# Optimization experiments

Hardware: AMD Instinct MI355X
Metric: run time of the kernel (lower is better)

The kernel has to match this reference:

```python
import jax, jax.numpy as jnp
import numpy as np

N_NODES = 50000


def _sage_conv(x, src, dst, W_l, b_l, W_r, n_nodes):
    # mean-aggregate neighbor (source) features onto targets
    msg = x[src]                                   # [E, d_in] gather
    agg = jax.ops.segment_sum(msg, dst, num_segments=n_nodes)   # [N, d_in]
    deg = jax.ops.segment_sum(jnp.ones((src.shape[0],), x.dtype), dst,
                              num_segments=n_nodes)
    agg = agg / jnp.clip(deg, 1.0, None)[:, None]  # mean with deg>=1 clamp (PyG)
    # out = lin_l(agg) + lin_r(x)   (bias lives in lin_l)
    return agg @ W_l.T + b_l + x @ W_r.T


def setup_inputs() -> dict:
    key = jax.random.key(0)
    ks = jax.random.split(key, 8)
    d_in, d_hid, d_out = 128, 256, 128
    n_edges = 800000
    x = jax.random.normal(ks[0], (N_NODES, d_in), dtype=jnp.float32)
    edge_index = jax.random.randint(ks[1], (2, n_edges), 0, N_NODES, dtype=jnp.int32)
    def glorot(k, shape):
        lim = float(np.sqrt(6.0 / (shape[0] + shape[1])))
        return jax.random.uniform(k, shape, jnp.float32, -lim, lim)
    return {
        "x": x,
        "edge_index": edge_index,
        "W1l": glorot(ks[2], (d_hid, d_in)),
        "b1": jnp.zeros((d_hid,), jnp.float32),
        "W1r": glorot(ks[3], (d_hid, d_in)),
        "W2l": glorot(ks[4], (d_out, d_hid)),
        "b2": jnp.zeros((d_out,), jnp.float32),
        "W2r": glorot(ks[5], (d_out, d_hid)),
    }


def reference(x, edge_index, W1l, b1, W1r, W2l, b2, W2r):
    src, dst = edge_index[0], edge_index[1]
    h = jax.nn.relu(_sage_conv(x, src, dst, W1l, b1, W1r, N_NODES))
    out = _sage_conv(h, src, dst, W2l, b2, W2r, N_NODES)
    return out
```

## Files before the change

kernel.cpp:

```cpp
#include <hip/hip_runtime.h>
#include <hip/hip_bf16.h>

#define NN 50000
#define NN_PAD 50176
#define NE 800000
#define NB 196
#define CAP 6144
#define EPB 4096

typedef __attribute__((ext_vector_type(8))) short short8;
typedef __attribute__((ext_vector_type(4))) float f32x4;
typedef __attribute__((ext_vector_type(2))) float f32x2;

__device__ __forceinline__ unsigned short f2bf(float f) {
    union { float f; unsigned u; } v; v.f = f;
    unsigned u = v.u;
    return (unsigned short)((u + 0x7fffu + ((u >> 16) & 1u)) >> 16);
}
__device__ __forceinline__ float bfu_lo(unsigned u) {
    union { unsigned u; float f; } v; v.u = u << 16; return v.f;
}
__device__ __forceinline__ float bfu_hi(unsigned u) {
    union { unsigned u; float f; } v; v.u = u & 0xffff0000u; return v.f;
}

__global__ void k_setup_part(const float* __restrict__ W1l, const float* __restrict__ W1r,
                             const float* __restrict__ W2l, const float* __restrict__ W2r,
                             unsigned short* __restrict__ W1pk, unsigned short* __restrict__ W2pk,
                             const float4* __restrict__ x4, unsigned short* __restrict__ Abar1,
                             unsigned char* __restrict__ x_f8,
                             const int* __restrict__ src, const int* __restrict__ dst,
                             int* __restrict__ gcursor, unsigned* __restrict__ pairs) {
    int blk = blockIdx.x, t = threadIdx.x;
    if (blk < NB) {
        __shared__ int cnt[256];
        __shared__ int base[256];
        cnt[t] = 0;
        __syncthreads();
        int e0 = blk * EPB;
        int eend = min(e0 + EPB, NE);
        int rank[16], bk[16];
        unsigned pk[16];
        int m = 0;
        for (int e = e0 + t; e < eend; e += 256) {
            int s = src[e], d = dst[e];
            bk[m] = d >> 8;
            pk[m] = ((unsigned)s << 8) | (unsigned)(d & 255);
            rank[m] = atomicAdd(&cnt[bk[m]], 1);
            ++m;
        }
        __syncthreads();
        if (t < NB && cnt[t] > 0) base[t] = t * CAP + atomicAdd(&gcursor[t], cnt[t]);
        __syncthreads();
        for (int i = 0; i < m; ++i) {
            int pos = base[bk[i]] + rank[i];
            if (pos < (bk[i] + 1) * CAP) pairs[pos] = pk[i];
        }
    } else if (blk < 260) {
        int tid = (blk - 196) * 256 + t;
        int table = tid >> 13;
        int r = tid & 8191;
        int lane = r & 63, ni = (r >> 6) & 3, ks = (r >> 8) & 7, g = r >> 11;
        int lm = lane & 15, lq = lane >> 4;
        int o = g * 64 + ni * 16 + lm;
        int k = ks * 32 + lq * 8;
        unsigned short v[8];
        if (table == 0) {
            if (k < 128) {
#pragma unroll
                for (int j = 0; j < 8; ++j) v[j] = f2bf(W1l[o * 128 + k + j]);
            } else {
#pragma unroll
                for (int j = 0; j < 8; ++j) v[j] = f2bf(W1r[o * 128 + k - 128 + j]);
            }
            *(uint4*)(W1pk + (size_t)r * 8) = *(const uint4*)v;
        } else {
            if (o < 128) {
#pragma unroll
                for (int j = 0; j < 8; ++j) v[j] = f2bf(W2l[o * 256 + k + j]);
            } else {
#pragma unroll
                for (int j = 0; j < 8; ++j) v[j] = f2bf(W2r[(o - 128) * 256 + k + j]);
            }
            *(uint4*)(W2pk + (size_t)r * 8) = *(const uint4*)v;
        }
    } else {
        int gid = (blk - 260) * 256 + t;
        int n = gid >> 5, c = gid & 31;
        float4 v = x4[(size_t)n * 32 + c];
        ushort4 o;
        o.x = f2bf(v.x); o.y = f2bf(v.y); o.z = f2bf(v.z); o.w = f2bf(v.w);
        *(ushort4*)(Abar1 + (size_t)n * 256 + 128 + c * 4) = o;
        unsigned p = (unsigned)__builtin_amdgcn_cvt_pk_fp8_f32(v.x, v.y, 0, false);
        p = (unsigned)__builtin_amdgcn_cvt_pk_fp8_f32(v.z, v.w, (int)p, true);
        *(unsigned*)(x_f8 + (size_t)n * 128 + c * 4) = p;
    }
}

__global__ void k_build(const int* __restrict__ gcursor, const unsigned* __restrict__ pairs,
                        int* __restrict__ deg_i, int* __restrict__ row_start,
                        int* __restrict__ esrc) {
    __shared__ int buf[256];
    __shared__ int ldeg[256];
    __shared__ int lstart[256];
    __shared__ int sh_base, sh_cnt;
    __shared__ int lsrc[CAP];
    int b = blockIdx.x, t = threadIdx.x;
    int c = (t < NB) ? min(gcursor[t], CAP) : 0;
    buf[t] = c;
    __syncthreads();
#pragma unroll
    for (int o = 1; o < 256; o <<= 1) {
        int add = (t >= o) ? buf[t - o] : 0;
        __syncthreads();
        buf[t] += add;
        __syncthreads();
    }
    if (t == b) { sh_cnt = c; sh_base = buf[b] - c; }
    ldeg[t] = 0;
    __syncthreads();
    int cnt = sh_cnt, base = sh_base;
    int rank[CAP / 256], msrc[CAP / 256], mloc[CAP / 256];
    int m = 0;
    for (int e = t; e < cnt; e += 256) {
        unsigned p = pairs[(size_t)b * CAP + e];
        msrc[m] = (int)(p >> 8); mloc[m] = (int)(p & 255u);
        rank[m] = atomicAdd(&ldeg[mloc[m]], 1);
        ++m;
    }
    __syncthreads();
    int v = ldeg[t];
    buf[t] = v;
    __syncthreads();
#pragma unroll
    for (int o = 1; o < 256; o <<= 1) {
        int add = (t >= o) ? buf[t - o] : 0;
        __syncthreads();
        buf[t] += add;
        __syncthreads();
    }
    lstart[t] = buf[t] - v;
    int node = b * 256 + t;
    if (node < NN) { deg_i[node] = v; row_start[node] = base + lstart[t]; }
    else           { deg_i[node] = 0; row_start[node] = 0; }
    __syncthreads();
    for (int i = 0; i < m; ++i) lsrc[lstart[mloc[i]] + rank[i]] = msrc[i];
    __syncthreads();
    for (int e = t; e < cnt; e += 256) esrc[base + e] = lsrc[e];
}

__global__ void k_agg1(const uint2* __restrict__ xf8, const int* __restrict__ deg_i,
                       const int* __restrict__ row_start, const int* __restrict__ esrc,
                       unsigned short* __restrict__ Abar1) {
    int gid = blockIdx.x * blockDim.x + threadIdx.x;
    int n = gid >> 4, c = gid & 15;
    int dg = deg_i[n], st = row_start[n];
    float acc[8] = {0.f, 0.f, 0.f, 0.f, 0.f, 0.f, 0.f, 0.f};
    int i = 0;
    for (; i + 2 <= dg; i += 2) {
        int s0 = esrc[st + i], s1 = esrc[st + i + 1];
        uint2 q0 = xf8[(size_t)s0 * 16 + c];
        uint2 q1 = xf8[(size_t)s1 * 16 + c];
        f32x2 a0 = __builtin_amdgcn_cvt_pk_f32_fp8(q0.x, false);
        f32x2 a1 = __builtin_amdgcn_cvt_pk_f32_fp8(q0.x, true);
        f32x2 a2 = __builtin_amdgcn_cvt_pk_f32_fp8(q0.y, false);
        f32x2 a3 = __builtin_amdgcn_cvt_pk_f32_fp8(q0.y, true);
        f32x2 b0 = __builtin_amdgcn_cvt_pk_f32_fp8(q1.x, false);
        f32x2 b1 = __builtin_amdgcn_cvt_pk_f32_fp8(q1.x, true);
        f32x2 b2 = __builtin_amdgcn_cvt_pk_f32_fp8(q1.y, false);
        f32x2 b3 = __builtin_amdgcn_cvt_pk_f32_fp8(q1.y, true);
        acc[0] += a0.x + b0.x; acc[1] += a0.y + b0.y;
        acc[2] += a1.x + b1.x; acc[3] += a1.y + b1.y;
        acc[4] += a2.x + b2.x; acc[5] += a2.y + b2.y;
        acc[6] += a3.x + b3.x; acc[7] += a3.y + b3.y;
    }
    if (i < dg) {
        int s = esrc[st + i];
        uint2 q0 = xf8[(size_t)s * 16 + c];
        f32x2 a0 = __builtin_amdgcn_cvt_pk_f32_fp8(q0.x, false);
        f32x2 a1 = __builtin_amdgcn_cvt_pk_f32_fp8(q0.x, true);
        f32x2 a2 = __builtin_amdgcn_cvt_pk_f32_fp8(q0.y, false);
        f32x2 a3 = __builtin_amdgcn_cvt_pk_f32_fp8(q0.y, true);
        acc[0] += a0.x; acc[1] += a0.y;
        acc[2] += a1.x; acc[3] += a1.y;
        acc[4] += a2.x; acc[5] += a2.y;
        acc[6] += a3.x; acc[7] += a3.y;
    }
    float invd = 1.0f / (float)max(dg, 1);
    unsigned short o[8];
#pragma unroll
    for (int j = 0; j < 8; ++j) o[j] = f2bf(acc[j] * invd);
    *(uint4*)(Abar1 + (size_t)n * 256 + c * 8) = *(const uint4*)o;
}

__global__ __launch_bounds__(256, 2) void k_gemm12(
        const unsigned short* __restrict__ Abar1,
        const unsigned short* __restrict__ W1pk, const unsigned short* __restrict__ W2pk,
        const float* __restrict__ b1, const float* __restrict__ b2,
        unsigned char* __restrict__ y2f8, unsigned short* __restrict__ Sbf) {
    __shared__ unsigned short T[16384];
    int t = threadIdx.x, blk = blockIdx.x;
    int m0 = blk * 64;
    int wave = t >> 6, lane = t & 63;
    int lm = lane & 15, lq = lane >> 4;
    int pbase = lm * 4 + lq;

    short8 w[8][4];
    {
        const unsigned short* wb = W1pk + (size_t)wave * 16384;
#pragma unroll
        for (int ks = 0; ks < 8; ++ks)
#pragma unroll
            for (int ni = 0; ni < 4; ++ni)
                w[ks][ni] = *(const short8*)(wb + ((size_t)((ks * 4 + ni) * 64 + lane)) * 8);
    }

    {
        const uint4* gp = (const uint4*)(Abar1 + (size_t)m0 * 256);
        uint4 ld[8];
#pragma unroll
        for (int i = 0; i < 8; ++i) ld[i] = gp[i * 256 + t];
        int ks = (t >> 2) & 7, slq = t & 3;
#pragma unroll
        for (int i = 0; i < 8; ++i) {
            int mLoc = i * 8 + (t >> 5);
            int mi = mLoc >> 4, slm = mLoc & 15;
            *(uint4*)(T + ((size_t)((ks * 4 + mi) * 64 + slm * 4 + slq)) * 8) = ld[i];
        }
    }
    __syncthreads();

    f32x4 acc1[4][4];
#pragma unroll
    for (int mi = 0; mi < 4; ++mi)
#pragma unroll
        for (int ni = 0; ni < 4; ++ni) acc1[mi][ni] = (f32x4){0.f, 0.f, 0.f, 0.f};
#pragma unroll
    for (int ks = 0; ks < 8; ++ks) {
        short8 a[4];
#pragma unroll
        for (int mi = 0; mi < 4; ++mi)
            a[mi] = *(const short8*)(T + ((size_t)((ks * 4 + mi) * 64 + pbase)) * 8);
#pragma unroll
        for (int mi = 0; mi < 4; ++mi)
#pragma unroll
            for (int ni = 0; ni < 4; ++ni)
                acc1[mi][ni] = __builtin_amdgcn_mfma_f32_16x16x32_bf16(a[mi], w[ks][ni], acc1[mi][ni], 0, 0, 0);
    }

    {
        const unsigned short* wb = W2pk + (size_t)wave * 16384;
#pragma unroll
        for (int ks = 0; ks < 8; ++ks)
#pragma unroll
            for (int ni = 0; ni < 4; ++ni)
                w[ks][ni] = *(const short8*)(wb + ((size_t)((ks * 4 + ni) * 64 + lane)) * 8);
    }
    __syncthreads();

#pragma unroll
    for (int ni = 0; ni < 4; ++ni) {
        int col = wave * 64 + ni * 16 + lm;
        float bv = b1[col];
        int ks = col >> 5;
        int la = (col & 31) >> 3, j = col & 7;
#pragma unroll
        for (int mi = 0; mi < 4; ++mi)
#pragma unroll
            for (int r = 0; r < 4; ++r) {
                float v = fmaxf(acc1[mi][ni][r] + bv, 0.0f);
                T[((size_t)((ks * 4 + mi) * 64 + (lq * 4 + r) * 4 + la)) * 8 + j] = f2bf(v);
            }
    }
    __syncthreads();

    f32x4 acc2[4][4];
#pragma unroll
    for (int mi = 0; mi < 4; ++mi)
#pragma unroll
        for (int ni = 0; ni < 4; ++ni) acc2[mi][ni] = (f32x4){0.f, 0.f, 0.f, 0.f};
#pragma unroll
    for (int ks = 0; ks < 8; ++ks) {
        short8 a[4];
#pragma unroll
        for (int mi = 0; mi < 4; ++mi)
            a[mi] = *(const short8*)(T + ((size_t)((ks * 4 + mi) * 64 + pbase)) * 8);
#pragma unroll
        for (int mi = 0; mi < 4; ++mi)
#pragma unroll
            for (int ni = 0; ni < 4; ++ni)
                acc2[mi][ni] = __builtin_amdgcn_mfma_f32_16x16x32_bf16(a[mi], w[ks][ni], acc2[mi][ni], 0, 0, 0);
    }

    if (wave < 2) {
#pragma unroll
        for (int ni = 0; ni < 4; ++ni) {
            int col = wave * 64 + ni * 16 + lm;
#pragma unroll
            for (int mi = 0; mi < 4; ++mi)
#pragma unroll
                for (int r = 0; r < 4; ++r) {
                    int row = blk * 64 + mi * 16 + lq * 4 + r;
                    float v = acc2[mi][ni][r];
                    unsigned p = (unsigned)__builtin_amdgcn_cvt_pk_fp8_f32(v, v, 0, false);
                    y2f8[(size_t)row * 128 + col] = (unsigned char)(p & 0xff);
                }
        }
    } else {
#pragma unroll
        for (int ni = 0; ni < 4; ++ni) {
            int col = (wave - 2) * 64 + ni * 16 + lm;
            float bv = b2[col];
#pragma unroll
            for (int mi = 0; mi < 4; ++mi)
#pragma unroll
                for (int r = 0; r < 4; ++r) {
                    int row = blk * 64 + mi * 16 + lq * 4 + r;
                    Sbf[(size_t)row * 128 + col] = f2bf(acc2[mi][ni][r] + bv);
                }
        }
    }
}

__global__ void k_agg_out(const uint2* __restrict__ yf8, const uint4* __restrict__ Sbf4,
                          const int* __restrict__ deg_i, const int* __restrict__ row_start,
                          const int* __restrict__ esrc, float* __restrict__ out) {
    int gid = blockIdx.x * blockDim.x + threadIdx.x;
    int n = gid >> 4, c = gid & 15;
    int dg = deg_i[n], st = row_start[n];
    float acc[8] = {0.f, 0.f, 0.f, 0.f, 0.f, 0.f, 0.f, 0.f};
    int i = 0;
    for (; i + 2 <= dg; i += 2) {
        int s0 = esrc[st + i], s1 = esrc[st + i + 1];
        uint2 q0 = yf8[(size_t)s0 * 16 + c];
        uint2 q1 = yf8[(size_t)s1 * 16 + c];
        f32x2 a0 = __builtin_amdgcn_cvt_pk_f32_fp8(q0.x, false);
        f32x2 a1 = __builtin_amdgcn_cvt_pk_f32_fp8(q0.x, true);
        f32x2 a2 = __builtin_amdgcn_cvt_pk_f32_fp8(q0.y, false);
        f32x2 a3 = __builtin_amdgcn_cvt_pk_f32_fp8(q0.y, true);
        f32x2 b0 = __builtin_amdgcn_cvt_pk_f32_fp8(q1.x, false);
        f32x2 b1 = __builtin_amdgcn_cvt_pk_f32_fp8(q1.x, true);
        f32x2 b2 = __builtin_amdgcn_cvt_pk_f32_fp8(q1.y, false);
        f32x2 b3 = __builtin_amdgcn_cvt_pk_f32_fp8(q1.y, true);
        acc[0] += a0.x + b0.x; acc[1] += a0.y + b0.y;
        acc[2] += a1.x + b1.x; acc[3] += a1.y + b1.y;
        acc[4] += a2.x + b2.x; acc[5] += a2.y + b2.y;
        acc[6] += a3.x + b3.x; acc[7] += a3.y + b3.y;
    }
    if (i < dg) {
        int s = esrc[st + i];
        uint2 q0 = yf8[(size_t)s * 16 + c];
        f32x2 a0 = __builtin_amdgcn_cvt_pk_f32_fp8(q0.x, false);
        f32x2 a1 = __builtin_amdgcn_cvt_pk_f32_fp8(q0.x, true);
        f32x2 a2 = __builtin_amdgcn_cvt_pk_f32_fp8(q0.y, false);
        f32x2 a3 = __builtin_amdgcn_cvt_pk_f32_fp8(q0.y, true);
        acc[0] += a0.x; acc[1] += a0.y;
        acc[2] += a1.x; acc[3] += a1.y;
        acc[4] += a2.x; acc[5] += a2.y;
        acc[6] += a3.x; acc[7] += a3.y;
    }
    float invd = 1.0f / (float)max(dg, 1);
    uint4 sv = Sbf4[(size_t)n * 16 + c];
    float4 o0, o1;
    o0.x = bfu_lo(sv.x) + acc[0] * invd; o0.y = bfu_hi(sv.x) + acc[1] * invd;
    o0.z = bfu_lo(sv.y) + acc[2] * invd; o0.w = bfu_hi(sv.y) + acc[3] * invd;
    o1.x = bfu_lo(sv.z) + acc[4] * invd; o1.y = bfu_hi(sv.z) + acc[5] * invd;
    o1.z = bfu_lo(sv.w) + acc[6] * invd; o1.w = bfu_hi(sv.w) + acc[7] * invd;
    float* op = out + (size_t)n * 128 + c * 8;
    *(float4*)op = o0; *(float4*)(op + 4) = o1;
}

extern "C" void kernel_launch(void* const* d_in, const int* in_sizes, int n_in,
                              void* d_out, int out_size, void* d_ws, size_t ws_size,
                              hipStream_t stream) {
    const float* x   = (const float*)d_in[0];
    const int*   ei  = (const int*)d_in[1];
    const int*   src = ei;
    const int*   dst = ei + NE;
    const float* W1l = (const float*)d_in[2];
    const float* b1  = (const float*)d_in[3];
    const float* W1r = (const float*)d_in[4];
    const float* W2l = (const float*)d_in[5];
    const float* b2  = (const float*)d_in[6];
    const float* W2r = (const float*)d_in[7];
    float* out = (float*)d_out;

    char* ws = (char*)d_ws;
    int* deg_i            = (int*)(ws + 0);
    int* row_start        = (int*)(ws + 200704);
    int* gcursor          = (int*)(ws + 401408);
    int* esrc             = (int*)(ws + 409600);
    unsigned* pairs       = (unsigned*)(ws + 4194304);
    unsigned short* Sbf   = (unsigned short*)(ws + 9437184);
    unsigned char* x_f8   = (unsigned char*)(ws + 22282240);
    unsigned char* y2f8   = (unsigned char*)(ws + 28704768);
    unsigned short* Abar1 = (unsigned short*)(ws + 35651584);
    unsigned short* W1pk  = (unsigned short*)(ws + 61341696);
    unsigned short* W2pk  = (unsigned short*)(ws + 61472768);

    hipMemsetAsync(gcursor, 0, 1024, stream);
    k_setup_part<<<6510, 256, 0, stream>>>(W1l, W1r, W2l, W2r, W1pk, W2pk,
                                           (const float4*)x, Abar1, x_f8, src, dst,
                                           gcursor, pairs);
    k_build<<<NB, 256, 0, stream>>>(gcursor, pairs, deg_i, row_start, esrc);
    k_agg1<<<NN * 16 / 256, 256, 0, stream>>>((const uint2*)x_f8, deg_i, row_start, esrc, Abar1);
    k_gemm12<<<NN_PAD / 64, 256, 0, stream>>>(Abar1, W1pk, W2pk, b1, b2, y2f8, Sbf);
    k_agg_out<<<NN * 16 / 256, 256, 0, stream>>>((const uint2*)y2f8, (const uint4*)Sbf,
                                                 deg_i, row_start, esrc, out);
}
```

Baseline: 187.8 us.

## Compact CSR to 16-bit edge sources and packed start/degree metadata

Stores edge source indices as 16-bit values and packs each node's row start (20 bits) and degree (12 bits) into one word, so the aggregation kernels do one metadata load and move half the index bytes. The partition and build kernels become two-pass count-then-scatter loops with shared-memory cursors instead of keeping per-thread rank arrays in registers. The 16-bit LDS staging buffer also halves k_build's shared memory. The cost is rereading src/dst and pairs a second time, and the packing assumes node ids fit in 16 bits and degrees stay below 4096.

```diff
diff --git a/kernel.cpp b/kernel.cpp
--- a/kernel.cpp
+++ b/kernel.cpp
@@ -34,27 +34,22 @@
     int blk = blockIdx.x, t = threadIdx.x;
     if (blk < NB) {
         __shared__ int cnt[256];
+        __shared__ int cur[256];
         __shared__ int base[256];
-        cnt[t] = 0;
+        cnt[t] = 0; cur[t] = 0;
         __syncthreads();
         int e0 = blk * EPB;
         int eend = min(e0 + EPB, NE);
-        int rank[16], bk[16];
-        unsigned pk[16];
-        int m = 0;
+        for (int e = e0 + t; e < eend; e += 256)
+            atomicAdd(&cnt[dst[e] >> 8], 1);
+        __syncthreads();
+        if (t < NB && cnt[t] > 0) base[t] = t * CAP + atomicAdd(&gcursor[t], cnt[t]);
+        __syncthreads();
         for (int e = e0 + t; e < eend; e += 256) {
             int s = src[e], d = dst[e];
-            bk[m] = d >> 8;
-            pk[m] = ((unsigned)s << 8) | (unsigned)(d & 255);
-            rank[m] = atomicAdd(&cnt[bk[m]], 1);
-            ++m;
-        }
-        __syncthreads();
-        if (t < NB && cnt[t] > 0) base[t] = t * CAP + atomicAdd(&gcursor[t], cnt[t]);
-        __syncthreads();
-        for (int i = 0; i < m; ++i) {
-            int pos = base[bk[i]] + rank[i];
-            if (pos < (bk[i] + 1) * CAP) pairs[pos] = pk[i];
+            int bk = d >> 8;
+            int pos = base[bk] + atomicAdd(&cur[bk], 1);
+            if (pos < (bk + 1) * CAP) pairs[pos] = ((unsigned)s << 8) | (unsigned)(d & 255);
         }
     } else if (blk < 260) {
         int tid = (blk - 196) * 256 + t;
@@ -98,13 +93,12 @@
 }
 
 __global__ void k_build(const int* __restrict__ gcursor, const unsigned* __restrict__ pairs,
-                        int* __restrict__ deg_i, int* __restrict__ row_start,
-                        int* __restrict__ esrc) {
+                        unsigned* __restrict__ meta, unsigned short* __restrict__ esrc) {
     __shared__ int buf[256];
     __shared__ int ldeg[256];
-    __shared__ int lstart[256];
+    __shared__ int cur[256];
     __shared__ int sh_base, sh_cnt;
-    __shared__ int lsrc[CAP];
+    __shared__ unsigned short lsrc[CAP];
     int b = blockIdx.x, t = threadIdx.x;
     int c = (t < NB) ? min(gcursor[t], CAP) : 0;
     buf[t] = c;
@@ -120,41 +114,40 @@
     ldeg[t] = 0;
     __syncthreads();
     int cnt = sh_cnt, base = sh_base;
-    int rank[CAP / 256], msrc[CAP / 256], mloc[CAP / 256];
-    int m = 0;
+    for (int e = t; e < cnt; e += 256)
+        atomicAdd(&ldeg[pairs[(size_t)b * CAP + e] & 255u], 1);
+    __syncthreads();
+    int v = ldeg[t];
+    buf[t] = v;
+    __syncthreads();
+#pragma unroll
+    for (int o = 1; o < 256; o <<= 1) {
+        int add = (t >= o) ? buf[t - o] : 0;
+        __syncthreads();
+        buf[t] += add;
+        __syncthreads();
+    }
+    int lst = buf[t] - v;
+    cur[t] = lst;
+    int node = b * 256 + t;
+    meta[node] = (node < NN) ? ((unsigned)(base + lst) | ((unsigned)v << 20)) : 0u;
+    __syncthreads();
     for (int e = t; e < cnt; e += 256) {
         unsigned p = pairs[(size_t)b * CAP + e];
-        msrc[m] = (int)(p >> 8); mloc[m] = (int)(p & 255u);
-        rank[m] = atomicAdd(&ldeg[mloc[m]], 1);
-        ++m;
-    }
-    __syncthreads();
-    int v = ldeg[t];
-    buf[t] = v;
-    __syncthreads();
-#pragma unroll
-    for (int o = 1; o < 256; o <<= 1) {
-        int add = (t >= o) ? buf[t - o] : 0;
-        __syncthreads();
-        buf[t] += add;
-        __syncthreads();
-    }
-    lstart[t] = buf[t] - v;
-    int node = b * 256 + t;
-    if (node < NN) { deg_i[node] = v; row_start[node] = base + lstart[t]; }
-    else           { deg_i[node] = 0; row_start[node] = 0; }
-    __syncthreads();
-    for (int i = 0; i < m; ++i) lsrc[lstart[mloc[i]] + rank[i]] = msrc[i];
+        int pos = atomicAdd(&cur[p & 255u], 1);
+        lsrc[pos] = (unsigned short)(p >> 8);
+    }
     __syncthreads();
     for (int e = t; e < cnt; e += 256) esrc[base + e] = lsrc[e];
 }
 
-__global__ void k_agg1(const uint2* __restrict__ xf8, const int* __restrict__ deg_i,
-                       const int* __restrict__ row_start, const int* __restrict__ esrc,
+__global__ void k_agg1(const uint2* __restrict__ xf8, const unsigned* __restrict__ meta,
+                       const unsigned short* __restrict__ esrc,
                        unsigned short* __restrict__ Abar1) {
     int gid = blockIdx.x * blockDim.x + threadIdx.x;
     int n = gid >> 4, c = gid & 15;
-    int dg = deg_i[n], st = row_start[n];
+    unsigned mt = meta[n];
+    int st = (int)(mt & 0xFFFFFu), dg = (int)(mt >> 20);
     float acc[8] = {0.f, 0.f, 0.f, 0.f, 0.f, 0.f, 0.f, 0.f};
     int i = 0;
     for (; i + 2 <= dg; i += 2) {
@@ -323,11 +316,13 @@
 }
 
 __global__ void k_agg_out(const uint2* __restrict__ yf8, const uint4* __restrict__ Sbf4,
-                          const int* __restrict__ deg_i, const int* __restrict__ row_start,
-                          const int* __restrict__ esrc, float* __restrict__ out) {
+                          const unsigned* __restrict__ meta,
+                          const unsigned short* __restrict__ esrc,
+                          float* __restrict__ out) {
     int gid = blockIdx.x * blockDim.x + threadIdx.x;
     int n = gid >> 4, c = gid & 15;
-    int dg = deg_i[n], st = row_start[n];
+    unsigned mt = meta[n];
+    int st = (int)(mt & 0xFFFFFu), dg = (int)(mt >> 20);
     float acc[8] = {0.f, 0.f, 0.f, 0.f, 0.f, 0.f, 0.f, 0.f};
     int i = 0;
     for (; i + 2 <= dg; i += 2) {
@@ -386,10 +381,9 @@
     float* out = (float*)d_out;
 
     char* ws = (char*)d_ws;
-    int* deg_i            = (int*)(ws + 0);
-    int* row_start        = (int*)(ws + 200704);
+    unsigned* meta        = (unsigned*)(ws + 0);
     int* gcursor          = (int*)(ws + 401408);
-    int* esrc             = (int*)(ws + 409600);
+    unsigned short* esrc  = (unsigned short*)(ws + 409600);
     unsigned* pairs       = (unsigned*)(ws + 4194304);
     unsigned short* Sbf   = (unsigned short*)(ws + 9437184);
     unsigned char* x_f8   = (unsigned char*)(ws + 22282240);
@@ -402,9 +396,9 @@
     k_setup_part<<<6510, 256, 0, stream>>>(W1l, W1r, W2l, W2r, W1pk, W2pk,
                                            (const float4*)x, Abar1, x_f8, src, dst,
                                            gcursor, pairs);
-    k_build<<<NB, 256, 0, stream>>>(gcursor, pairs, deg_i, row_start, esrc);
-    k_agg1<<<NN * 16 / 256, 256, 0, stream>>>((const uint2*)x_f8, deg_i, row_start, esrc, Abar1);
+    k_build<<<NB, 256, 0, stream>>>(gcursor, pairs, meta, esrc);
+    k_agg1<<<NN * 16 / 256, 256, 0, stream>>>((const uint2*)x_f8, meta, esrc, Abar1);
     k_gemm12<<<NN_PAD / 64, 256, 0, stream>>>(Abar1, W1pk, W2pk, b1, b2, y2f8, Sbf);
     k_agg_out<<<NN * 16 / 256, 256, 0, stream>>>((const uint2*)y2f8, (const uint4*)Sbf,
-                                                 deg_i, row_start, esrc, out);
-}
+                                                 meta, esrc, out);
+}
```

After: 187.0 us. No clear change (-0.4%).
